# Optimization experiments

Hardware: AMD Instinct MI355X
Metric: run time of the kernel (lower is better)

The kernel has to match this reference:

```python
import jax, jax.numpy as jnp
import numpy as np

N = 8192        # num nodes == input_dim (attn is [N,N], indexed by edge endpoints)
E = 262144      # num edges (nnz of sparse G), avg degree 32
OD = 64         # output_dim


def setup_inputs() -> dict:
    key = jax.random.key(0)
    k_x, k_r, k_c, k_v, k_a, k_w = jax.random.split(key, 6)
    x = jax.random.normal(k_x, (N, N), dtype=jnp.float32)
    row = jax.random.randint(k_r, (E,), 0, N)
    col = jax.random.randint(k_c, (E,), 0, N)
    values = jax.random.uniform(k_v, (E,), dtype=jnp.float32)
    attn = jax.random.uniform(k_a, (N, N), dtype=jnp.float32)  # init uniform(0,1) per reset_parameters
    stdv = 1.0 / np.sqrt(OD)
    weight = jax.random.uniform(k_w, (N, OD), dtype=jnp.float32, minval=-stdv, maxval=stdv)
    return {"x": x, "attn": attn, "weight": weight, "values": values, "row": row, "col": col}


def reference(x, attn, weight, values, row, col):
    # x = x @ W : [N, OD]
    y = x @ weight
    # sparse_dense_mul: scale each edge's value by attn[row, col] (irregular gather)
    ev = values * attn[row, col]                      # [E]
    # torch.sparse.mm(G, y): out[i] = sum_{e: row[e]==i} ev[e] * y[col[e]]
    out = jax.ops.segment_sum(ev[:, None] * y[col], row, num_segments=x.shape[0])
    return (out, jnp.linalg.norm(attn))
```

## Files before the change

kernel.cpp:

```cpp
#include <hip/hip_runtime.h>
#include <hip/hip_bf16.h>

#define N 8192
#define OD 64
#define E_EDGES 262144

#define BM 64
#define KSPLIT 32
#define KSLICE (N / KSPLIT)
#define SCAT_BLOCKS 8192
#define EDGE_ITERS (E_EDGES / (SCAT_BLOCKS * 4))

typedef __attribute__((ext_vector_type(8))) short bf16x8;
typedef __attribute__((ext_vector_type(4))) float f32x4;

__device__ __forceinline__ unsigned short f2bf(float f) {
    union { float f; unsigned u; } v; v.f = f;
    unsigned r = (v.u + 0x7fffu + ((v.u >> 16) & 1u)) >> 16;
    return (unsigned short)r;
}

__device__ __forceinline__ unsigned pack_trunc(unsigned lo, unsigned hi) {
#if defined(__has_builtin) && __has_builtin(__builtin_amdgcn_perm)
    return __builtin_amdgcn_perm(hi, lo, 0x07060302u);
#else
    return (lo >> 16) | (hi & 0xFFFF0000u);
#endif
}

__device__ __forceinline__ void gload16(const void* g, void* l) {
    __builtin_amdgcn_global_load_lds(
        (const __attribute__((address_space(1))) unsigned int*)g,
        (__attribute__((address_space(3))) unsigned int*)l, 16, 0, 0);
}

__global__ __launch_bounds__(256) void prep_kernel(const float* __restrict__ w,
                                                   unsigned short* __restrict__ wt,
                                                   float4* __restrict__ y4,
                                                   float4* __restrict__ out4) {
    const int bid = blockIdx.x, t = threadIdx.x;
    const int base = bid * 256 + t;
    float4 z{0.f, 0.f, 0.f, 0.f};
    #pragma unroll
    for (int u = 0; u < 4; ++u) y4[base + u * 32768] = z;
    #pragma unroll
    for (int u = 0; u < 4; ++u) out4[base + u * 32768] = z;

    __shared__ unsigned short lds[64][80];
    const int kb = bid * 64;
    #pragma unroll
    for (int p = 0; p < 4; ++p) {
        int idx = p * 1024 + t * 4;
        int r = idx >> 6, c = idx & 63;
        float4 v = *(const float4*)(&w[(size_t)(kb + r) * OD + c]);
        lds[c + 0][r] = f2bf(v.x);
        lds[c + 1][r] = f2bf(v.y);
        lds[c + 2][r] = f2bf(v.z);
        lds[c + 3][r] = f2bf(v.w);
    }
    __syncthreads();
    const int colx = t >> 2, j0 = (t & 3) * 16;
    #pragma unroll
    for (int u = 0; u < 2; ++u) {
        *(bf16x8*)(wt + (size_t)colx * N + kb + j0 + u * 8) =
            *(const bf16x8*)(&lds[colx][j0 + u * 8]);
    }
}

__global__ __launch_bounds__(256) void gemm_kernel(const float* __restrict__ x,
                                                   const unsigned short* __restrict__ wt,
                                                   float* __restrict__ y) {
    __shared__ unsigned short blds[64 * KSLICE];

    const int t = threadIdx.x;
    const int wv = t >> 6, lane = t & 63;
    const int lrow = lane & 15, g = lane >> 4;
    const int row = blockIdx.x * BM + wv * 16 + lrow;
    const int k0 = blockIdx.y * KSLICE;
    const int key = (lrow & 7) << 3;

    const float* xp = x + (size_t)row * N + k0 + g * 8;
    uint4 xb[16];
    #pragma unroll
    for (int i = 0; i < 8; ++i) {
        xb[2 * i]     = *(const uint4*)(xp + i * 32);
        xb[2 * i + 1] = *(const uint4*)(xp + i * 32 + 4);
    }

    #pragma unroll
    for (int j = 0; j < 8; ++j) {
        const int idx = j * 256 + t;
        const int br = idx >> 5;
        const int ch = idx & 31;
        gload16(wt + (size_t)br * N + k0 + ((ch ^ (br & 7)) << 3),
                &blds[idx * 8]);
    }

    asm volatile("s_waitcnt vmcnt(0)" ::: "memory");
    __builtin_amdgcn_sched_barrier(0);
    __builtin_amdgcn_s_barrier();

    f32x4 acc[4] = {f32x4{0,0,0,0}, f32x4{0,0,0,0}, f32x4{0,0,0,0}, f32x4{0,0,0,0}};
    #pragma unroll
    for (int q = 0; q < 2; ++q) {
        bf16x8 A[4];
        #pragma unroll
        for (int i = 0; i < 4; ++i) {
            union { bf16x8 v; unsigned u[4]; } Au;
            Au.u[0] = pack_trunc(xb[q * 8 + 2 * i].x,     xb[q * 8 + 2 * i].y);
            Au.u[1] = pack_trunc(xb[q * 8 + 2 * i].z,     xb[q * 8 + 2 * i].w);
            Au.u[2] = pack_trunc(xb[q * 8 + 2 * i + 1].x, xb[q * 8 + 2 * i + 1].y);
            Au.u[3] = pack_trunc(xb[q * 8 + 2 * i + 1].z, xb[q * 8 + 2 * i + 1].w);
            A[i] = Au.v;
        }
        #pragma unroll
        for (int ks = 0; ks < 4; ++ks) {
            #pragma unroll
            for (int cf = 0; cf < 4; ++cf) {
                const int ko = q * 128 + ks * 32 + g * 8;
                bf16x8 b = *(const bf16x8*)&blds[(cf * 16 + lrow) * KSLICE + (ko ^ key)];
                acc[cf] = __builtin_amdgcn_mfma_f32_16x16x32_bf16(A[ks], b, acc[cf], 0, 0, 0);
            }
        }
    }

    float* yp = y + ((size_t)blockIdx.x * BM + wv * 16 + g * 4) * OD;
    #pragma unroll
    for (int cf = 0; cf < 4; ++cf) {
        #pragma unroll
        for (int i = 0; i < 4; ++i)
            atomicAdd(&yp[i * OD + cf * 16 + lrow], acc[cf][i]);
    }
}

__device__ __forceinline__ void do_scatter(const float* __restrict__ values,
                                           const float* __restrict__ attn,
                                           const int* __restrict__ row,
                                           const int* __restrict__ col,
                                           const float* __restrict__ y,
                                           float* __restrict__ out,
                                           int bid, int t) {
    const int lane = t & 63;
    const int w = t >> 6;
    int r8[EDGE_ITERS], c8[EDGE_ITERS];
    float v8[EDGE_ITERS], a8[EDGE_ITERS];
    #pragma unroll
    for (int i = 0; i < EDGE_ITERS; ++i) {
        int e = bid * 4 + w + i * (SCAT_BLOCKS * 4);
        r8[i] = row[e]; c8[i] = col[e]; v8[i] = values[e];
    }
    #pragma unroll
    for (int i = 0; i < EDGE_ITERS; ++i)
        a8[i] = attn[(size_t)r8[i] * N + c8[i]];
    #pragma unroll
    for (int i = 0; i < EDGE_ITERS; ++i) {
        float yv = y[c8[i] * OD + lane];
        atomicAdd(&out[r8[i] * OD + lane], v8[i] * a8[i] * yv);
    }
}

__device__ __forceinline__ float do_norm_part(const float* __restrict__ attn, int bid, int t) {
    const float4* a4 = (const float4*)attn;
    float s = 0.f;
    int i = bid * 256 + t;
    #pragma unroll
    for (int u = 0; u < 8; ++u) {
        float4 v = a4[i + u * (SCAT_BLOCKS * 256)];
        s += v.x * v.x + v.y * v.y + v.z * v.z + v.w * v.w;
    }
    return s;
}

__global__ __launch_bounds__(256) void scatter_norm_kernel(
        const float* __restrict__ values, const float* __restrict__ attn,
        const int* __restrict__ row, const int* __restrict__ col,
        const float* __restrict__ y, float* __restrict__ out,
        float* __restrict__ part) {
    const int bid = blockIdx.x, t = threadIdx.x;
    float s;
    if (bid & 1) {
        s = do_norm_part(attn, bid, t);
        do_scatter(values, attn, row, col, y, out, bid, t);
    } else {
        do_scatter(values, attn, row, col, y, out, bid, t);
        s = do_norm_part(attn, bid, t);
    }
    for (int off = 32; off > 0; off >>= 1) s += __shfl_down(s, off, 64);
    __shared__ float wpart[4];
    int wid = t >> 6;
    if ((t & 63) == 0) wpart[wid] = s;
    __syncthreads();
    if (t == 0) part[bid] = wpart[0] + wpart[1] + wpart[2] + wpart[3];
}

__global__ __launch_bounds__(256) void finalize_kernel(const float* __restrict__ part,
                                                       float* __restrict__ out_norm) {
    float s = 0.f;
    #pragma unroll
    for (int k = 0; k < SCAT_BLOCKS / 256; ++k) s += part[k * 256 + threadIdx.x];
    for (int off = 32; off > 0; off >>= 1) s += __shfl_down(s, off, 64);
    __shared__ float wp[4];
    int wid = threadIdx.x >> 6;
    if ((threadIdx.x & 63) == 0) wp[wid] = s;
    __syncthreads();
    if (threadIdx.x == 0) *out_norm = sqrtf(wp[0] + wp[1] + wp[2] + wp[3]);
}

extern "C" void kernel_launch(void* const* d_in, const int* in_sizes, int n_in,
                              void* d_out, int out_size, void* d_ws, size_t ws_size,
                              hipStream_t stream) {
    const float* x      = (const float*)d_in[0];
    const float* attn   = (const float*)d_in[1];
    const float* weight = (const float*)d_in[2];
    const float* values = (const float*)d_in[3];
    const int*   row    = (const int*)d_in[4];
    const int*   col    = (const int*)d_in[5];
    float* out = (float*)d_out;

    char* wsb = (char*)d_ws;
    float*          part = (float*)wsb;
    unsigned short* wt   = (unsigned short*)(wsb + (1u << 20));
    float*          y    = (float*)(wsb + (2u << 20));

    prep_kernel<<<128, 256, 0, stream>>>(weight, wt, (float4*)y, (float4*)out);
    gemm_kernel<<<dim3(N / BM, KSPLIT), 256, 0, stream>>>(x, wt, y);
    scatter_norm_kernel<<<SCAT_BLOCKS, 256, 0, stream>>>(values, attn, row, col, y, out, part);
    finalize_kernel<<<1, 256, 0, stream>>>(part, out + (size_t)N * OD);
}
```

Before: 159.3 us.

## Move attn norm into GEMM launch and fold finalize into scatter

The Frobenius-norm partial sums over attn now run in every third block of the GEMM launch, which interleaves 2048 norm blocks with the 4096 GEMM blocks. The scatter kernel no longer streams attn for the norm and gains one extra block that reduces the partials and writes the sqrt, so the separate finalize launch is gone. The aim is to overlap the bandwidth-bound norm read with the GEMM and leave the latency-bound scatter on its own. The cost is a heavier GEMM phase, and the finalize block could be scheduled before other scatter blocks, though its partials come from the earlier launch.

```diff
diff --git a/kernel.cpp b/kernel.cpp
--- a/kernel.cpp
+++ b/kernel.cpp
@@ -8,6 +8,7 @@
 #define BM 64
 #define KSPLIT 32
 #define KSLICE (N / KSPLIT)
+#define NORM_BLOCKS 2048
 #define SCAT_BLOCKS 8192
 #define EDGE_ITERS (E_EDGES / (SCAT_BLOCKS * 4))
 
@@ -67,16 +68,40 @@
     }
 }
 
-__global__ __launch_bounds__(256) void gemm_kernel(const float* __restrict__ x,
-                                                   const unsigned short* __restrict__ wt,
-                                                   float* __restrict__ y) {
+__global__ __launch_bounds__(256) void gemm_norm_kernel(const float* __restrict__ x,
+                                                        const unsigned short* __restrict__ wt,
+                                                        float* __restrict__ y,
+                                                        const float* __restrict__ attn,
+                                                        float* __restrict__ part) {
     __shared__ unsigned short blds[64 * KSLICE];
-
-    const int t = threadIdx.x;
+    const int bid = blockIdx.x, t = threadIdx.x;
+
+    if ((bid % 3) == 2) {
+        const int ni = bid / 3;
+        const float4* a4 = (const float4*)attn;
+        const long nbase = (long)ni * 8192;
+        float s = 0.f;
+        #pragma unroll 8
+        for (int u = 0; u < 32; ++u) {
+            float4 v = a4[nbase + u * 256 + t];
+            s += v.x * v.x + v.y * v.y + v.z * v.z + v.w * v.w;
+        }
+        for (int off = 32; off > 0; off >>= 1) s += __shfl_down(s, off, 64);
+        __shared__ float wpart[4];
+        int wid = t >> 6;
+        if ((t & 63) == 0) wpart[wid] = s;
+        __syncthreads();
+        if (t == 0) part[ni] = wpart[0] + wpart[1] + wpart[2] + wpart[3];
+        return;
+    }
+
+    const int gi = (bid / 3) * 2 + (bid % 3);
+    const int bx = gi & 127;
+    const int by = gi >> 7;
     const int wv = t >> 6, lane = t & 63;
     const int lrow = lane & 15, g = lane >> 4;
-    const int row = blockIdx.x * BM + wv * 16 + lrow;
-    const int k0 = blockIdx.y * KSLICE;
+    const int row = bx * BM + wv * 16 + lrow;
+    const int k0 = by * KSLICE;
     const int key = (lrow & 7) << 3;
 
     const float* xp = x + (size_t)row * N + k0 + g * 8;
@@ -124,7 +149,7 @@
         }
     }
 
-    float* yp = y + ((size_t)blockIdx.x * BM + wv * 16 + g * 4) * OD;
+    float* yp = y + ((size_t)bx * BM + wv * 16 + g * 4) * OD;
     #pragma unroll
     for (int cf = 0; cf < 4; ++cf) {
         #pragma unroll
@@ -133,13 +158,28 @@
     }
 }
 
-__device__ __forceinline__ void do_scatter(const float* __restrict__ values,
-                                           const float* __restrict__ attn,
-                                           const int* __restrict__ row,
-                                           const int* __restrict__ col,
-                                           const float* __restrict__ y,
-                                           float* __restrict__ out,
-                                           int bid, int t) {
+__global__ __launch_bounds__(256) void scatter_kernel(const float* __restrict__ values,
+                                                      const float* __restrict__ attn,
+                                                      const int* __restrict__ row,
+                                                      const int* __restrict__ col,
+                                                      const float* __restrict__ y,
+                                                      float* __restrict__ out,
+                                                      const float* __restrict__ part,
+                                                      float* __restrict__ out_norm) {
+    const int t = threadIdx.x;
+    if (blockIdx.x == SCAT_BLOCKS) {
+        float s = 0.f;
+        #pragma unroll
+        for (int k = 0; k < NORM_BLOCKS / 256; ++k) s += part[k * 256 + t];
+        for (int off = 32; off > 0; off >>= 1) s += __shfl_down(s, off, 64);
+        __shared__ float wp[4];
+        int wid = t >> 6;
+        if ((t & 63) == 0) wp[wid] = s;
+        __syncthreads();
+        if (t == 0) *out_norm = sqrtf(wp[0] + wp[1] + wp[2] + wp[3]);
+        return;
+    }
+    const int bid = blockIdx.x;
     const int lane = t & 63;
     const int w = t >> 6;
     int r8[EDGE_ITERS], c8[EDGE_ITERS];
@@ -157,53 +197,6 @@
         float yv = y[c8[i] * OD + lane];
         atomicAdd(&out[r8[i] * OD + lane], v8[i] * a8[i] * yv);
     }
-}
-
-__device__ __forceinline__ float do_norm_part(const float* __restrict__ attn, int bid, int t) {
-    const float4* a4 = (const float4*)attn;
-    float s = 0.f;
-    int i = bid * 256 + t;
-    #pragma unroll
-    for (int u = 0; u < 8; ++u) {
-        float4 v = a4[i + u * (SCAT_BLOCKS * 256)];
-        s += v.x * v.x + v.y * v.y + v.z * v.z + v.w * v.w;
-    }
-    return s;
-}
-
-__global__ __launch_bounds__(256) void scatter_norm_kernel(
-        const float* __restrict__ values, const float* __restrict__ attn,
-        const int* __restrict__ row, const int* __restrict__ col,
-        const float* __restrict__ y, float* __restrict__ out,
-        float* __restrict__ part) {
-    const int bid = blockIdx.x, t = threadIdx.x;
-    float s;
-    if (bid & 1) {
-        s = do_norm_part(attn, bid, t);
-        do_scatter(values, attn, row, col, y, out, bid, t);
-    } else {
-        do_scatter(values, attn, row, col, y, out, bid, t);
-        s = do_norm_part(attn, bid, t);
-    }
-    for (int off = 32; off > 0; off >>= 1) s += __shfl_down(s, off, 64);
-    __shared__ float wpart[4];
-    int wid = t >> 6;
-    if ((t & 63) == 0) wpart[wid] = s;
-    __syncthreads();
-    if (t == 0) part[bid] = wpart[0] + wpart[1] + wpart[2] + wpart[3];
-}
-
-__global__ __launch_bounds__(256) void finalize_kernel(const float* __restrict__ part,
-                                                       float* __restrict__ out_norm) {
-    float s = 0.f;
-    #pragma unroll
-    for (int k = 0; k < SCAT_BLOCKS / 256; ++k) s += part[k * 256 + threadIdx.x];
-    for (int off = 32; off > 0; off >>= 1) s += __shfl_down(s, off, 64);
-    __shared__ float wp[4];
-    int wid = threadIdx.x >> 6;
-    if ((threadIdx.x & 63) == 0) wp[wid] = s;
-    __syncthreads();
-    if (threadIdx.x == 0) *out_norm = sqrtf(wp[0] + wp[1] + wp[2] + wp[3]);
 }
 
 extern "C" void kernel_launch(void* const* d_in, const int* in_sizes, int n_in,
@@ -223,7 +216,7 @@
     float*          y    = (float*)(wsb + (2u << 20));
 
     prep_kernel<<<128, 256, 0, stream>>>(weight, wt, (float4*)y, (float4*)out);
-    gemm_kernel<<<dim3(N / BM, KSPLIT), 256, 0, stream>>>(x, wt, y);
-    scatter_norm_kernel<<<SCAT_BLOCKS, 256, 0, stream>>>(values, attn, row, col, y, out, part);
-    finalize_kernel<<<1, 256, 0, stream>>>(part, out + (size_t)N * OD);
-}
+    gemm_norm_kernel<<<6144, 256, 0, stream>>>(x, wt, y, attn, part);
+    scatter_kernel<<<SCAT_BLOCKS + 1, 256, 0, stream>>>(values, attn, row, col, y, out,
+                                                        part, out + (size_t)N * OD);
+}
```

Result: slower. 171.0 us (+7.3%).
